# Performance work log

Measured on AMD Instinct MI355X. Metric: run time of the kernel, lower is better.

The kernel has to match this reference:

```python
import jax, jax.numpy as jnp
import numpy as np

B, T, F, H, L = 256, 512, 64, 256, 2
DH = 2 * H          # decoder hidden size (bidirectional encoder concat)
OUT, OSL = 2, 20    # output_size, output_seq_len


def gru_cell(x, h, Wih, Whh, bih, bhh):
    # PyTorch GRU cell, gate order (r, z, n)
    gi = x @ Wih.T + bih
    gh = h @ Whh.T + bhh
    ir, iz, inn = jnp.split(gi, 3, axis=-1)
    hr, hz, hn = jnp.split(gh, 3, axis=-1)
    r = jax.nn.sigmoid(ir + hr)
    z = jax.nn.sigmoid(iz + hz)
    n = jnp.tanh(inn + r * hn)
    return (1.0 - z) * n + z * h


def setup_inputs() -> dict:
    key = jax.random.key(0)
    ks = iter(jax.random.split(key, 32))
    def p(shape, scale=0.05):
        return jax.random.normal(next(ks), shape, dtype=jnp.float32) * scale
    inp = {
        "x": p((B, T, F), 1.0),
        "start_token": jnp.zeros((1, 1, OUT), jnp.float32),
        # encoder layer 0 (input F), layer 1 (input 2H); axis 0 = direction (fwd, bwd)
        "enc_Wih0": p((2, 3 * H, F)), "enc_Whh0": p((2, 3 * H, H)),
        "enc_bih0": p((2, 3 * H)),   "enc_bhh0": p((2, 3 * H)),
        "enc_Wih1": p((2, 3 * H, 2 * H)), "enc_Whh1": p((2, 3 * H, H)),
        "enc_bih1": p((2, 3 * H)),   "enc_bhh1": p((2, 3 * H)),
        # decoder: unidirectional, hidden DH; layer0 input OUT, layer1 input DH
        "dec_Wih0": p((3 * DH, OUT)), "dec_Whh0": p((3 * DH, DH)),
        "dec_bih0": p((3 * DH,)),    "dec_bhh0": p((3 * DH,)),
        "dec_Wih1": p((3 * DH, DH)), "dec_Whh1": p((3 * DH, DH)),
        "dec_bih1": p((3 * DH,)),    "dec_bhh1": p((3 * DH,)),
        "fc_W": p((OUT, DH)), "fc_b": p((OUT,)),
    }
    return inp


def _run_dir(xs, Wih, Whh, bih, bhh, reverse):
    # xs: [T, B, Fin] -> (ys [T, B, H], h_T [B, H])
    h0 = jnp.zeros((xs.shape[1], Whh.shape[1]), xs.dtype)
    def step(h, xt):
        hn = gru_cell(xt, h, Wih, Whh, bih, bhh)
        return hn, hn
    hT, ys = jax.lax.scan(step, h0, xs, reverse=reverse)
    return ys, hT


def reference(x, start_token,
              enc_Wih0, enc_Whh0, enc_bih0, enc_bhh0,
              enc_Wih1, enc_Whh1, enc_bih1, enc_bhh1,
              dec_Wih0, dec_Whh0, dec_bih0, dec_bhh0,
              dec_Wih1, dec_Whh1, dec_bih1, dec_bhh1,
              fc_W, fc_b):
    b = x.shape[0]
    xs = jnp.swapaxes(x, 0, 1)  # [T, B, F]
    enc_layers = [(enc_Wih0, enc_Whh0, enc_bih0, enc_bhh0),
                  (enc_Wih1, enc_Whh1, enc_bih1, enc_bhh1)]
    hiddens = []
    layer_in = xs
    for (Wih, Whh, bih, bhh) in enc_layers:
        yf, hf = _run_dir(layer_in, Wih[0], Whh[0], bih[0], bhh[0], reverse=False)
        yb, hb = _run_dir(layer_in, Wih[1], Whh[1], bih[1], bhh[1], reverse=True)
        layer_in = jnp.concatenate([yf, yb], axis=-1)   # [T, B, 2H]
        hiddens.append(jnp.concatenate([hf, hb], axis=-1))  # [B, 2H] = cat(fwd, bwd)
    inp0 = jnp.broadcast_to(start_token, (b, 1, OUT))[:, 0]  # [B, OUT]
    def dec_step(carry, _):
        inp, (h0, h1) = carry
        h0n = gru_cell(inp, h0, dec_Wih0, dec_Whh0, dec_bih0, dec_bhh0)
        h1n = gru_cell(h0n, h1, dec_Wih1, dec_Whh1, dec_bih1, dec_bhh1)
        pred = h1n @ fc_W.T + fc_b
        return (pred, (h0n, h1n)), pred
    _, preds = jax.lax.scan(dec_step, (inp0, (hiddens[0], hiddens[1])), None, length=OSL)
    return jnp.swapaxes(preds, 0, 1)  # [B, OSL, OUT]
```

## Files before the change

kernel.cpp:

```cpp
#include <hip/hip_runtime.h>
#include <hip/hip_bf16.h>
#include <stdint.h>
#include <stddef.h>


typedef __bf16 bf16_t;
typedef bf16_t bf16x8 __attribute__((ext_vector_type(8)));
typedef float  f32x4  __attribute__((ext_vector_type(4)));

#define B_   256
#define T_   512
#define F_   64
#define H_   256
#define G_   768
#define DH_  512
#define DG_  1536
#define OSL_ 20

__device__ __forceinline__ float sigm(float x) {
    float e = __builtin_amdgcn_exp2f(-1.442695040888963f * x);
    return __builtin_amdgcn_rcpf(1.0f + e);
}
__device__ __forceinline__ float tanh_(float x) {
    float e = __builtin_amdgcn_exp2f(-2.885390081777927f * x);
    return __builtin_amdgcn_rcpf(1.0f + e) * 2.0f - 1.0f;
}

__device__ __forceinline__ bf16x8 load_f32x8_as_bf16(const float* p) {
    f32x4 u = *(const f32x4*)p;
    f32x4 v = *(const f32x4*)(p + 4);
    bf16x8 r;
    r[0]=(bf16_t)u[0]; r[1]=(bf16_t)u[1]; r[2]=(bf16_t)u[2]; r[3]=(bf16_t)u[3];
    r[4]=(bf16_t)v[0]; r[5]=(bf16_t)v[1]; r[6]=(bf16_t)v[2]; r[7]=(bf16_t)v[3];
    return r;
}

__global__ __launch_bounds__(256) void prep_all(
    const float* __restrict__ s0, const float* __restrict__ s1,
    const float* __restrict__ s2, const float* __restrict__ s3,
    const float* __restrict__ s4, const float* __restrict__ s5,
    const float* __restrict__ s6,
    bf16_t* __restrict__ d0, bf16_t* __restrict__ d1, bf16_t* __restrict__ d2,
    bf16_t* __restrict__ d3, bf16_t* __restrict__ d4, bf16_t* __restrict__ d5,
    bf16_t* __restrict__ d6,
    const float* __restrict__ wih0d, const float* __restrict__ fcw,
    const float* __restrict__ fcb, const float* __restrict__ bih0d,
    const float* __restrict__ st, bf16_t* __restrict__ weff,
    float* __restrict__ beff, float* __restrict__ ov,
    unsigned int* __restrict__ bar) {
    int i = blockIdx.x * 256 + threadIdx.x;
    switch (blockIdx.y) {
      case 0: if (i < 2*G_*F_)  d0[i] = (bf16_t)s0[i]; break;
      case 1: if (i < 2*G_*H_)  d1[i] = (bf16_t)s1[i]; break;
      case 2: if (i < 2*G_*DH_) d2[i] = (bf16_t)s2[i]; break;
      case 3: if (i < 2*G_*H_)  d3[i] = (bf16_t)s3[i]; break;
      case 4: if (i < DG_*DH_)  d4[i] = (bf16_t)s4[i]; break;
      case 5: if (i < DG_*DH_)  d5[i] = (bf16_t)s5[i]; break;
      case 6: if (i < DG_*DH_)  d6[i] = (bf16_t)s6[i]; break;
      default: {
        if (i < 1024) bar[i] = 0u;
        if (i < DG_*DH_) {
          int g = i >> 9, k = i & 511;
          float a0 = wih0d[g * 2], a1 = wih0d[g * 2 + 1];
          weff[i] = (bf16_t)(a0 * fcw[k] + a1 * fcw[DH_ + k]);
          if (k == 0) {
            beff[g] = a0 * fcb[0] + a1 * fcb[1] + bih0d[g];
            ov[g]   = a0 * st[0]  + a1 * st[1]  + bih0d[g];
          }
        }
      } break;
    }
}

__global__ __launch_bounds__(256) void gemm_gi(
    const float* __restrict__ x, const bf16_t* __restrict__ xcat,
    const bf16_t* __restrict__ Bt, bf16_t* __restrict__ gi, int t0, int K) {
    __shared__ bf16_t As[128 * 64];
    __shared__ bf16_t Bs[128 * 64];
    int m0 = blockIdx.x * 128, n0 = blockIdx.y * 128;
    int tid = threadIdx.x;
    int lane = tid & 63, w = tid >> 6;
    int col = lane & 15, quad = lane >> 4;
    int qm = (w >> 1) * 64, qn = (w & 1) * 64;

    int tl = m0 >> 8;
    int bbase = m0 & 255;
    int t_real = t0 + tl;
    if (n0 >= 768) t_real = (T_ - 1) - t_real;

    f32x4 acc[4][4] = {};
    for (int k0 = 0; k0 < K; k0 += 64) {
        __syncthreads();
#pragma unroll
        for (int i = 0; i < 4; i++) {
            int c = i * 256 + tid;
            int m = c >> 3, kc = c & 7;
            int kcs = kc ^ (m & 7);
            bf16x8 av;
            if (K == 64) {
                av = load_f32x8_as_bf16(x + ((size_t)(bbase + m) * T_ + t_real) * F_ + kcs * 8);
            } else {
                av = *(const bf16x8*)(xcat + ((size_t)t_real * B_ + bbase + m) * DH_ + k0 + kcs * 8);
            }
            *(bf16x8*)(&As[c * 8]) = av;
            *(bf16x8*)(&Bs[c * 8]) = *(const bf16x8*)(Bt + (size_t)(n0 + m) * K + k0 + kcs * 8);
        }
        __syncthreads();
#pragma unroll
        for (int kt = 0; kt < 2; kt++) {
            bf16x8 a[4], b[4];
#pragma unroll
            for (int mt = 0; mt < 4; mt++) {
                int r = qm + mt * 16 + col;
                a[mt] = *(const bf16x8*)(&As[(r * 8 + ((kt * 4 + quad) ^ (r & 7))) * 8]);
                int rn = qn + mt * 16 + col;
                b[mt] = *(const bf16x8*)(&Bs[(rn * 8 + ((kt * 4 + quad) ^ (rn & 7))) * 8]);
            }
#pragma unroll
            for (int mt = 0; mt < 4; mt++)
#pragma unroll
                for (int nt = 0; nt < 4; nt++)
                    acc[mt][nt] = __builtin_amdgcn_mfma_f32_16x16x32_bf16(a[mt], b[nt], acc[mt][nt], 0, 0, 0);
        }
    }
#pragma unroll
    for (int mt = 0; mt < 4; mt++)
#pragma unroll
        for (int nt = 0; nt < 4; nt++)
#pragma unroll
            for (int i = 0; i < 4; i++) {
                int row = m0 + qm + mt * 16 + quad * 4 + i;
                int cg  = n0 + qn + nt * 16 + col;
                gi[(size_t)row * DG_ + cg] = (bf16_t)acc[mt][nt][i];
            }
}

__global__ __launch_bounds__(512) void gru_scan(
    const bf16_t* __restrict__ gi, int t0, int tc,
    const bf16_t* __restrict__ whh,
    const float* __restrict__ bih, const float* __restrict__ bhh,
    float* __restrict__ hstate, bf16_t* __restrict__ y, float* __restrict__ hT) {
    __shared__ bf16_t gi_lds[16 * 768];
    __shared__ bf16_t h_lds[2 * 16 * 264];

    int dir = blockIdx.x >> 4;
    int b0  = (blockIdx.x & 15) * 16;
    int tid = threadIdx.x;
    int w = tid >> 6, lane = tid & 63, col = lane & 15, quad = lane >> 4;

    bf16x8 wf[3][2][8];
    const bf16_t* wbase = whh + (size_t)dir * G_ * H_;
#pragma unroll
    for (int g = 0; g < 3; g++)
#pragma unroll
        for (int nt = 0; nt < 2; nt++) {
            int row = g * 256 + w * 32 + nt * 16 + col;
#pragma unroll
            for (int kt = 0; kt < 8; kt++)
                wf[g][nt][kt] = *(const bf16x8*)(wbase + (size_t)row * H_ + kt * 32 + quad * 8);
        }
    float brz[2][2], bin_[2], bhn[2];
#pragma unroll
    for (int nt = 0; nt < 2; nt++) {
        int j = w * 32 + nt * 16 + col;
        brz[0][nt] = bih[dir * G_ + j] + bhh[dir * G_ + j];
        brz[1][nt] = bih[dir * G_ + 256 + j] + bhh[dir * G_ + 256 + j];
        bin_[nt]   = bih[dir * G_ + 512 + j];
        bhn[nt]    = bhh[dir * G_ + 512 + j];
    }
    int bb[3], oo[3];
#pragma unroll
    for (int it = 0; it < 3; it++) {
        int c = it * 512 + tid;
        bb[it] = c / 96;
        oo[it] = (c % 96) * 8;
    }
    float hold[2][4];
#pragma unroll
    for (int nt = 0; nt < 2; nt++)
#pragma unroll
        for (int i = 0; i < 4; i++) {
            int j = w * 32 + nt * 16 + col;
            hold[nt][i] = t0 ? hstate[dir * 65536 + (b0 + quad * 4 + i) * 256 + j] : 0.0f;
        }
    for (int i = tid; i < 16 * 264; i += 512) {
        int b = i / 264, j = i % 264;
        float v = (t0 && j < 256) ? hstate[dir * 65536 + (b0 + b) * 256 + j] : 0.0f;
        h_lds[i] = (bf16_t)v;
    }
#pragma unroll
    for (int it = 0; it < 3; it++) {
        int c = it * 512 + tid;
        *(bf16x8*)(&gi_lds[c * 8]) =
            *(const bf16x8*)(gi + ((size_t)0 * B_ + b0 + bb[it]) * DG_ + dir * G_ + oo[it]);
    }
    __syncthreads();

    for (int s = 0; s < tc; s++) {
        int par = s & 1;
        int t = t0 + s;
        int sn = (s + 1 < tc) ? (s + 1) : s;

        bf16x8 pg[3];
#pragma unroll
        for (int it = 0; it < 3; it++)
            pg[it] = *(const bf16x8*)(gi + ((size_t)sn * B_ + b0 + bb[it]) * DG_ + dir * G_ + oo[it]);

        f32x4 acc[3][2] = {};
        const bf16_t* hcur = &h_lds[par * 4224];
#pragma unroll
        for (int kt = 0; kt < 8; kt++) {
            bf16x8 af = *(const bf16x8*)(hcur + col * 264 + kt * 32 + quad * 8);
#pragma unroll
            for (int g = 0; g < 3; g++)
#pragma unroll
                for (int nt = 0; nt < 2; nt++)
                    acc[g][nt] = __builtin_amdgcn_mfma_f32_16x16x32_bf16(af, wf[g][nt][kt], acc[g][nt], 0, 0, 0);
        }

        bf16_t* hnext = &h_lds[(par ^ 1) * 4224];
        int tp = dir ? (T_ - 1 - t) : t;
#pragma unroll
        for (int nt = 0; nt < 2; nt++) {
            int j = w * 32 + nt * 16 + col;
#pragma unroll
            for (int i = 0; i < 4; i++) {
                int b = quad * 4 + i;
                float gr = acc[0][nt][i] + (float)gi_lds[b * 768 + j]       + brz[0][nt];
                float gz = acc[1][nt][i] + (float)gi_lds[b * 768 + 256 + j] + brz[1][nt];
                float gn = (float)gi_lds[b * 768 + 512 + j] + bin_[nt];
                float r = sigm(gr), z = sigm(gz);
                float n = tanh_(gn + r * (acc[2][nt][i] + bhn[nt]));
                float hv = (1.0f - z) * n + z * hold[nt][i];
                hold[nt][i] = hv;
                hnext[b * 264 + j] = (bf16_t)hv;
                if (y) y[((size_t)tp * B_ + b0 + b) * DH_ + dir * H_ + j] = (bf16_t)hv;
                if (t == T_ - 1) hT[(size_t)(b0 + b) * DH_ + dir * H_ + j] = hv;
            }
        }
        __syncthreads();
#pragma unroll
        for (int it = 0; it < 3; it++)
            *(bf16x8*)(&gi_lds[(it * 512 + tid) * 8]) = pg[it];
        __syncthreads();
    }
#pragma unroll
    for (int nt = 0; nt < 2; nt++)
#pragma unroll
        for (int i = 0; i < 4; i++) {
            int j = w * 32 + nt * 16 + col;
            hstate[dir * 65536 + (b0 + quad * 4 + i) * 256 + j] = hold[nt][i];
        }
}


__device__ __forceinline__ void gbar(unsigned int* cnt) {
    __syncthreads();
    if (threadIdx.x == 0) {
        __hip_atomic_fetch_add(cnt, 1u, __ATOMIC_RELAXED, __HIP_MEMORY_SCOPE_AGENT);
        unsigned int s = 0;
        while (__hip_atomic_load(cnt, __ATOMIC_RELAXED, __HIP_MEMORY_SCOPE_AGENT) < 8u
               && ++s < (1u << 20))
            __builtin_amdgcn_s_sleep(1);
    }
    __syncthreads();
}

__device__ __forceinline__ void stage16_x(bf16_t* lds, const bf16_t* src) {
    f32x4 v0, v1, v2, v3;
    const char* s = (const char*)src;
    const char* a0 = s + threadIdx.x * 16;
    asm volatile(
        "global_load_dwordx4 %0, %4, off sc0 sc1\n\t"
        "global_load_dwordx4 %1, %5, off sc0 sc1\n\t"
        "global_load_dwordx4 %2, %6, off sc0 sc1\n\t"
        "global_load_dwordx4 %3, %7, off sc0 sc1\n\t"
        "s_waitcnt vmcnt(0)"
        : "=&v"(v0), "=&v"(v1), "=&v"(v2), "=&v"(v3)
        : "v"(a0), "v"(a0 + 4096), "v"(a0 + 8192), "v"(a0 + 12288)
        : "memory");
    f32x4 vv[4] = { v0, v1, v2, v3 };
#pragma unroll
    for (int i2 = 0; i2 < 4; ++i2) {
        int off = i2 * 4096 + threadIdx.x * 16;
        int row = off >> 10;
        int swz = off ^ ((row & 7) << 4);
        *(f32x4*)((char*)lds + swz) = vv[i2];
    }
}

__device__ __forceinline__ bf16x8 fragrd(const bf16_t* lds, int kt, int col, int quad) {
    int byte = (col * 1024 + kt * 64 + quad * 16) ^ ((col & 7) << 4);
    return *(const bf16x8*)((const char*)lds + byte);
}

__device__ __forceinline__ void publish(bf16_t* dst, int b, int j, float hv, int col) {
    bf16_t hb = (bf16_t)hv;
    unsigned short mb;
    __builtin_memcpy(&mb, &hb, 2);
    unsigned int pv = (unsigned int)__shfl_xor((int)(unsigned int)mb, 1);
    if ((col & 1) == 0) {
        unsigned int word = (unsigned int)mb | (pv << 16);
        void* addr = (char*)dst + (size_t)(b * DH_ + j) * 2;
        asm volatile("global_store_dword %0, %1, off sc0 sc1"
                     :: "v"(addr), "v"(word) : "memory");
    }
}

__device__ __forceinline__ void cell_step(
    const bf16_t* sh, const bf16_t* sx, bool dox,
    const bf16_t* __restrict__ Wx, const bf16_t* __restrict__ Wh,
    int j, int col, int quad, int grp,
    float br, float bz, float bin_, float bhn,
    float hold[4], bf16_t* hout, float* hist_t) {
    f32x4 aR = {}, aZ = {}, aIN = {}, aHN = {};
#pragma unroll
    for (int kt = 0; kt < 16; ++kt) {
        bf16x8 ah = fragrd(sh, kt, col, quad);
        bf16x8 w0 = *(const bf16x8*)(Wh + (size_t)j * DH_ + kt * 32 + quad * 8);
        bf16x8 w1 = *(const bf16x8*)(Wh + (size_t)(DH_ + j) * DH_ + kt * 32 + quad * 8);
        bf16x8 w2 = *(const bf16x8*)(Wh + (size_t)(2 * DH_ + j) * DH_ + kt * 32 + quad * 8);
        aR  = __builtin_amdgcn_mfma_f32_16x16x32_bf16(ah, w0, aR, 0, 0, 0);
        aZ  = __builtin_amdgcn_mfma_f32_16x16x32_bf16(ah, w1, aZ, 0, 0, 0);
        aHN = __builtin_amdgcn_mfma_f32_16x16x32_bf16(ah, w2, aHN, 0, 0, 0);
        if (dox) {
            bf16x8 ax = fragrd(sx, kt, col, quad);
            bf16x8 x0 = *(const bf16x8*)(Wx + (size_t)j * DH_ + kt * 32 + quad * 8);
            bf16x8 x1 = *(const bf16x8*)(Wx + (size_t)(DH_ + j) * DH_ + kt * 32 + quad * 8);
            bf16x8 x2 = *(const bf16x8*)(Wx + (size_t)(2 * DH_ + j) * DH_ + kt * 32 + quad * 8);
            aR  = __builtin_amdgcn_mfma_f32_16x16x32_bf16(ax, x0, aR, 0, 0, 0);
            aZ  = __builtin_amdgcn_mfma_f32_16x16x32_bf16(ax, x1, aZ, 0, 0, 0);
            aIN = __builtin_amdgcn_mfma_f32_16x16x32_bf16(ax, x2, aIN, 0, 0, 0);
        }
    }
#pragma unroll
    for (int i = 0; i < 4; ++i) {
        int b = grp * 16 + quad * 4 + i;
        float r = sigm(aR[i] + br);
        float z = sigm(aZ[i] + bz);
        float n = tanh_(aIN[i] + bin_ + r * (aHN[i] + bhn));
        float hv = (1.0f - z) * n + z * hold[i];
        hold[i] = hv;
        if (hist_t) hist_t[(size_t)b * DH_ + j] = hv;
        publish(hout, b, j, hv, col);
    }
}

__global__ __launch_bounds__(256) void dec_persist(
    const bf16_t* __restrict__ weff, const float* __restrict__ beff,
    const float* __restrict__ ov,
    const bf16_t* __restrict__ wdhh0, const float* __restrict__ dbhh0,
    const bf16_t* __restrict__ wdih1, const float* __restrict__ dbih1,
    const bf16_t* __restrict__ wdhh1, const float* __restrict__ dbhh1,
    const float* __restrict__ h0init, const float* __restrict__ h1init,
    bf16_t* hx00, bf16_t* hx01, bf16_t* hx10, bf16_t* hx11,
    float* __restrict__ hist, unsigned int* __restrict__ bar) {
    __shared__ bf16_t sh[16 * 512];
    __shared__ bf16_t sx[16 * 512];
    int jblk = blockIdx.x & 7;
    int grp  = blockIdx.x >> 3;
    int tid = threadIdx.x, w = tid >> 6, lane = tid & 63;
    int col = lane & 15, quad = lane >> 4;
    int j = jblk * 64 + w * 16 + col;

    float b0r = beff[j] + dbhh0[j],           b0z = beff[DH_ + j] + dbhh0[DH_ + j];
    float b0in = beff[2 * DH_ + j],           b0hn = dbhh0[2 * DH_ + j];
    float o0r = ov[j] + dbhh0[j],             o0z = ov[DH_ + j] + dbhh0[DH_ + j];
    float o0in = ov[2 * DH_ + j];
    float b1r = dbih1[j] + dbhh1[j],          b1z = dbih1[DH_ + j] + dbhh1[DH_ + j];
    float b1in = dbih1[2 * DH_ + j],          b1hn = dbhh1[2 * DH_ + j];

    float hold0[4], hold1[4];
#pragma unroll
    for (int i = 0; i < 4; ++i) {
        int b = grp * 16 + quad * 4 + i;
        float v0 = h0init[(size_t)b * DH_ + j];
        float v1 = h1init[(size_t)b * DH_ + j];
        hold0[i] = v0; hold1[i] = v1;
        publish(hx01, b, j, v0, col);
        publish(hx11, b, j, v1, col);
    }
    gbar(bar + grp);

    int ph = 1;
    for (int t = 0; t < OSL_; ++t) {
        bf16_t* write0 = (t & 1) ? hx01 : hx00;
        bf16_t* read0  = (t & 1) ? hx00 : hx01;
        bf16_t* write1 = (t & 1) ? hx11 : hx10;
        bf16_t* read1  = (t & 1) ? hx10 : hx11;
        bool dox0 = (t > 0);

        if (t == 0) stage16_x(sh, read0 + (size_t)grp * 16 * DH_);
        stage16_x(sx, read1 + (size_t)grp * 16 * DH_);
        __syncthreads();
        cell_step(sh, sx, dox0, weff, wdhh0, j, col, quad, grp,
                  dox0 ? b0r : o0r, dox0 ? b0z : o0z, dox0 ? b0in : o0in, b0hn,
                  hold0, write0, nullptr);
        gbar(bar + ph * 16 + grp); ph++;

        stage16_x(sh, write0 + (size_t)grp * 16 * DH_);
        __syncthreads();
        cell_step(sx, sh, true, wdih1, wdhh1, j, col, quad, grp,
                  b1r, b1z, b1in, b1hn,
                  hold1, write1, hist + (size_t)t * B_ * DH_);
        if (t < OSL_ - 1) { gbar(bar + ph * 16 + grp); ph++; }
    }
}

__global__ __launch_bounds__(256) void fc_all(
    const float* __restrict__ hist, const float* __restrict__ fcw,
    const float* __restrict__ fcb, float* __restrict__ out) {
    int t  = blockIdx.x >> 4;
    int b0 = (blockIdx.x & 15) * 16;
    int tid = threadIdx.x;
    int bl = tid >> 4, o = (tid >> 3) & 1, part = tid & 7;
    const float* hp = hist + ((size_t)t * B_ + b0 + bl) * DH_;
    const float* wp = fcw + o * DH_;
    float s = 0.0f;
    for (int k = part * 64; k < part * 64 + 64; k += 4) {
        f32x4 hv = *(const f32x4*)(hp + k);
        f32x4 wv = *(const f32x4*)(wp + k);
        s += hv[0] * wv[0] + hv[1] * wv[1] + hv[2] * wv[2] + hv[3] * wv[3];
    }
    s += __shfl_down(s, 4); s += __shfl_down(s, 2); s += __shfl_down(s, 1);
    if (part == 0) out[(size_t)(b0 + bl) * (OSL_ * 2) + t * 2 + o] = s + fcb[o];
}


#define OFF_WIH0E 0ull
#define OFF_WHH0E 196608ull
#define OFF_WIH1E 983040ull
#define OFF_WHH1E 2555904ull
#define OFF_WDHH0 3342336ull
#define OFF_WDIH1 4915200ull
#define OFF_WDHH1 6488064ull
#define OFF_WEFF  8060928ull
#define OFF_BEFF  9633792ull
#define OFF_BAR   9641984ull
#define OFF_OV    9658368ull
#define OFF_H0A   9682944ull
#define OFF_H0B   10207232ull
#define OFF_H1A   10731520ull
#define OFF_H1B   11255808ull
#define OFF_HST   11780096ull
#define OFF_HIST  12304384ull
#define OFF_XCAT  22790144ull
#define OFF_GI    157007872ull

extern "C" void kernel_launch(void* const* d_in, const int* in_sizes, int n_in,
                              void* d_out, int out_size, void* d_ws, size_t ws_size,
                              hipStream_t stream) {
    const float* x      = (const float*)d_in[0];
    const float* st     = (const float*)d_in[1];
    const float* eWih0  = (const float*)d_in[2];
    const float* eWhh0  = (const float*)d_in[3];
    const float* ebih0  = (const float*)d_in[4];
    const float* ebhh0  = (const float*)d_in[5];
    const float* eWih1  = (const float*)d_in[6];
    const float* eWhh1  = (const float*)d_in[7];
    const float* ebih1  = (const float*)d_in[8];
    const float* ebhh1  = (const float*)d_in[9];
    const float* dWih0  = (const float*)d_in[10];
    const float* dWhh0  = (const float*)d_in[11];
    const float* dbih0  = (const float*)d_in[12];
    const float* dbhh0  = (const float*)d_in[13];
    const float* dWih1  = (const float*)d_in[14];
    const float* dWhh1  = (const float*)d_in[15];
    const float* dbih1  = (const float*)d_in[16];
    const float* dbhh1  = (const float*)d_in[17];
    const float* fcW    = (const float*)d_in[18];
    const float* fcb    = (const float*)d_in[19];

    char* ws = (char*)d_ws;
    bf16_t* wih0e = (bf16_t*)(ws + OFF_WIH0E);
    bf16_t* whh0e = (bf16_t*)(ws + OFF_WHH0E);
    bf16_t* wih1e = (bf16_t*)(ws + OFF_WIH1E);
    bf16_t* whh1e = (bf16_t*)(ws + OFF_WHH1E);
    bf16_t* wdhh0 = (bf16_t*)(ws + OFF_WDHH0);
    bf16_t* wdih1 = (bf16_t*)(ws + OFF_WDIH1);
    bf16_t* wdhh1 = (bf16_t*)(ws + OFF_WDHH1);
    bf16_t* weff  = (bf16_t*)(ws + OFF_WEFF);
    float*  beff  = (float*)(ws + OFF_BEFF);
    unsigned int* bar = (unsigned int*)(ws + OFF_BAR);
    float*  ovp   = (float*)(ws + OFF_OV);
    float*  h0init = (float*)(ws + OFF_H0A);
    float*  h1init = (float*)(ws + OFF_H1A);
    bf16_t* hx00  = (bf16_t*)(ws + OFF_H0B);
    bf16_t* hx01  = (bf16_t*)(ws + OFF_H0B + 262144ull);
    bf16_t* hx10  = (bf16_t*)(ws + OFF_H1B);
    bf16_t* hx11  = (bf16_t*)(ws + OFF_H1B + 262144ull);
    float*  hstate = (float*)(ws + OFF_HST);
    float*  hist  = (float*)(ws + OFF_HIST);
    bf16_t* xcat  = (bf16_t*)(ws + OFF_XCAT);
    bf16_t* gi    = (bf16_t*)(ws + OFF_GI);

    int Tc = 512;
    while (Tc > 8 && OFF_GI + (unsigned long long)Tc * 786432ull > (unsigned long long)ws_size)
        Tc >>= 1;
    int nch = T_ / Tc;

    prep_all<<<dim3(3072, 8), 256, 0, stream>>>(
        eWih0, eWhh0, eWih1, eWhh1, dWhh0, dWih1, dWhh1,
        wih0e, whh0e, wih1e, whh1e, wdhh0, wdih1, wdhh1,
        dWih0, fcW, fcb, dbih0, st, weff, beff, ovp, bar);

    for (int c = 0; c < nch; c++) {
        gemm_gi<<<dim3(Tc * 2, 12), 256, 0, stream>>>(x, nullptr, wih0e, gi, c * Tc, 64);
        gru_scan<<<32, 512, 0, stream>>>(gi, c * Tc, Tc, whh0e, ebih0, ebhh0, hstate, xcat, h0init);
    }
    for (int c = 0; c < nch; c++) {
        gemm_gi<<<dim3(Tc * 2, 12), 256, 0, stream>>>(nullptr, xcat, wih1e, gi, c * Tc, 512);
        gru_scan<<<32, 512, 0, stream>>>(gi, c * Tc, Tc, whh1e, ebih1, ebhh1, hstate, nullptr, h1init);
    }

    dec_persist<<<128, 256, 0, stream>>>(weff, beff, ovp,
                                         wdhh0, dbhh0, wdih1, dbih1, wdhh1, dbhh1,
                                         h0init, h1init,
                                         hx00, hx01, hx10, hx11,
                                         hist, bar);

    fc_all<<<OSL_ * 16, 256, 0, stream>>>(hist, fcW, fcb, (float*)d_out);
}
```

Measured before the change: 4.631 ms.

## Hold decoder weights in registers and split gates across waves in persistent decoder

The persistent decoder kernel now runs 256 blocks of 512 threads. Each block owns 32 hidden columns, and each wave preloads one gate/matrix weight slice into registers once, instead of re-reading the weights from global memory on every step. Partial MFMA results are exchanged through LDS, and two waves apply the gate nonlinearities. The group barrier now expects 16 blocks per batch group. This trades global weight traffic per step for high register pressure (48 bf16x8 fragments per thread), extra LDS exchanges and syncs, and more blocks joining each barrier, with only 2 of 8 waves doing the elementwise work.

```diff
diff --git a/kernel.cpp b/kernel.cpp
--- a/kernel.cpp
+++ b/kernel.cpp
@@ -254,38 +254,39 @@
 }
 
 
-__device__ __forceinline__ void gbar(unsigned int* cnt) {
+__device__ __forceinline__ void gbar16(unsigned int* cnt) {
     __syncthreads();
     if (threadIdx.x == 0) {
         __hip_atomic_fetch_add(cnt, 1u, __ATOMIC_RELAXED, __HIP_MEMORY_SCOPE_AGENT);
         unsigned int s = 0;
-        while (__hip_atomic_load(cnt, __ATOMIC_RELAXED, __HIP_MEMORY_SCOPE_AGENT) < 8u
+        while (__hip_atomic_load(cnt, __ATOMIC_RELAXED, __HIP_MEMORY_SCOPE_AGENT) < 16u
                && ++s < (1u << 20))
             __builtin_amdgcn_s_sleep(1);
     }
     __syncthreads();
 }
 
-__device__ __forceinline__ void stage16_x(bf16_t* lds, const bf16_t* src) {
-    f32x4 v0, v1, v2, v3;
-    const char* s = (const char*)src;
-    const char* a0 = s + threadIdx.x * 16;
+__device__ __forceinline__ void stage16v(bf16_t* lds, const bf16_t* src) {
+    f32x4 v0, v1;
+    const char* a0 = (const char*)src + threadIdx.x * 16;
     asm volatile(
-        "global_load_dwordx4 %0, %4, off sc0 sc1\n\t"
-        "global_load_dwordx4 %1, %5, off sc0 sc1\n\t"
-        "global_load_dwordx4 %2, %6, off sc0 sc1\n\t"
-        "global_load_dwordx4 %3, %7, off sc0 sc1\n\t"
+        "global_load_dwordx4 %0, %2, off sc0 sc1\n\t"
+        "global_load_dwordx4 %1, %3, off sc0 sc1\n\t"
         "s_waitcnt vmcnt(0)"
-        : "=&v"(v0), "=&v"(v1), "=&v"(v2), "=&v"(v3)
-        : "v"(a0), "v"(a0 + 4096), "v"(a0 + 8192), "v"(a0 + 12288)
+        : "=&v"(v0), "=&v"(v1)
+        : "v"(a0), "v"(a0 + 8192)
         : "memory");
-    f32x4 vv[4] = { v0, v1, v2, v3 };
-#pragma unroll
-    for (int i2 = 0; i2 < 4; ++i2) {
-        int off = i2 * 4096 + threadIdx.x * 16;
+    {
+        int off = threadIdx.x * 16;
         int row = off >> 10;
         int swz = off ^ ((row & 7) << 4);
-        *(f32x4*)((char*)lds + swz) = vv[i2];
+        *(f32x4*)((char*)lds + swz) = v0;
+    }
+    {
+        int off = 8192 + threadIdx.x * 16;
+        int row = off >> 10;
+        int swz = off ^ ((row & 7) << 4);
+        *(f32x4*)((char*)lds + swz) = v1;
     }
 }
 
@@ -307,46 +308,7 @@
     }
 }
 
-__device__ __forceinline__ void cell_step(
-    const bf16_t* sh, const bf16_t* sx, bool dox,
-    const bf16_t* __restrict__ Wx, const bf16_t* __restrict__ Wh,
-    int j, int col, int quad, int grp,
-    float br, float bz, float bin_, float bhn,
-    float hold[4], bf16_t* hout, float* hist_t) {
-    f32x4 aR = {}, aZ = {}, aIN = {}, aHN = {};
-#pragma unroll
-    for (int kt = 0; kt < 16; ++kt) {
-        bf16x8 ah = fragrd(sh, kt, col, quad);
-        bf16x8 w0 = *(const bf16x8*)(Wh + (size_t)j * DH_ + kt * 32 + quad * 8);
-        bf16x8 w1 = *(const bf16x8*)(Wh + (size_t)(DH_ + j) * DH_ + kt * 32 + quad * 8);
-        bf16x8 w2 = *(const bf16x8*)(Wh + (size_t)(2 * DH_ + j) * DH_ + kt * 32 + quad * 8);
-        aR  = __builtin_amdgcn_mfma_f32_16x16x32_bf16(ah, w0, aR, 0, 0, 0);
-        aZ  = __builtin_amdgcn_mfma_f32_16x16x32_bf16(ah, w1, aZ, 0, 0, 0);
-        aHN = __builtin_amdgcn_mfma_f32_16x16x32_bf16(ah, w2, aHN, 0, 0, 0);
-        if (dox) {
-            bf16x8 ax = fragrd(sx, kt, col, quad);
-            bf16x8 x0 = *(const bf16x8*)(Wx + (size_t)j * DH_ + kt * 32 + quad * 8);
-            bf16x8 x1 = *(const bf16x8*)(Wx + (size_t)(DH_ + j) * DH_ + kt * 32 + quad * 8);
-            bf16x8 x2 = *(const bf16x8*)(Wx + (size_t)(2 * DH_ + j) * DH_ + kt * 32 + quad * 8);
-            aR  = __builtin_amdgcn_mfma_f32_16x16x32_bf16(ax, x0, aR, 0, 0, 0);
-            aZ  = __builtin_amdgcn_mfma_f32_16x16x32_bf16(ax, x1, aZ, 0, 0, 0);
-            aIN = __builtin_amdgcn_mfma_f32_16x16x32_bf16(ax, x2, aIN, 0, 0, 0);
-        }
-    }
-#pragma unroll
-    for (int i = 0; i < 4; ++i) {
-        int b = grp * 16 + quad * 4 + i;
-        float r = sigm(aR[i] + br);
-        float z = sigm(aZ[i] + bz);
-        float n = tanh_(aIN[i] + bin_ + r * (aHN[i] + bhn));
-        float hv = (1.0f - z) * n + z * hold[i];
-        hold[i] = hv;
-        if (hist_t) hist_t[(size_t)b * DH_ + j] = hv;
-        publish(hout, b, j, hv, col);
-    }
-}
-
-__global__ __launch_bounds__(256) void dec_persist(
+__global__ __launch_bounds__(512, 2) void dec_persist(
     const bf16_t* __restrict__ weff, const float* __restrict__ beff,
     const float* __restrict__ ov,
     const bf16_t* __restrict__ wdhh0, const float* __restrict__ dbhh0,
@@ -357,30 +319,52 @@
     float* __restrict__ hist, unsigned int* __restrict__ bar) {
     __shared__ bf16_t sh[16 * 512];
     __shared__ bf16_t sx[16 * 512];
-    int jblk = blockIdx.x & 7;
-    int grp  = blockIdx.x >> 3;
+    __shared__ f32x4 exch[12 * 64];
+
+    int s  = blockIdx.x & 15;
+    int g  = blockIdx.x >> 4;
+    int js = s * 32;
     int tid = threadIdx.x, w = tid >> 6, lane = tid & 63;
     int col = lane & 15, quad = lane >> 4;
-    int j = jblk * 64 + w * 16 + col;
-
-    float b0r = beff[j] + dbhh0[j],           b0z = beff[DH_ + j] + dbhh0[DH_ + j];
-    float b0in = beff[2 * DH_ + j],           b0hn = dbhh0[2 * DH_ + j];
-    float o0r = ov[j] + dbhh0[j],             o0z = ov[DH_ + j] + dbhh0[DH_ + j];
-    float o0in = ov[2 * DH_ + j];
-    float b1r = dbih1[j] + dbhh1[j],          b1z = dbih1[DH_ + j] + dbhh1[DH_ + j];
-    float b1in = dbih1[2 * DH_ + j],          b1hn = dbhh1[2 * DH_ + j];
+
+    const bf16_t* mats[4] = { wdhh0, weff, wdih1, wdhh1 };
+    bf16x8 frg[3][16];
+    int tmat[3], texch[3];
+#pragma unroll
+    for (int sl = 0; sl < 3; ++sl) {
+        int idx = w + sl * 8;
+        int m = idx / 6, rem = idx - m * 6;
+        int gate = rem >> 1, jh = rem & 1;
+        tmat[sl] = m;
+        texch[sl] = (m & 1) * 6 + rem;
+        int row = gate * 512 + js + jh * 16 + col;
+        const bf16_t* M = mats[m];
+#pragma unroll
+        for (int kt = 0; kt < 16; ++kt)
+            frg[sl][kt] = *(const bf16x8*)(M + (size_t)row * DH_ + kt * 32 + quad * 8);
+    }
+
+    int je = js + (w & 1) * 16 + col;
+    float b0r = beff[je] + dbhh0[je],        b0z = beff[DH_ + je] + dbhh0[DH_ + je];
+    float b0in = beff[2 * DH_ + je],         b0hn = dbhh0[2 * DH_ + je];
+    float o0r = ov[je] + dbhh0[je],          o0z = ov[DH_ + je] + dbhh0[DH_ + je];
+    float o0in = ov[2 * DH_ + je];
+    float b1r = dbih1[je] + dbhh1[je],       b1z = dbih1[DH_ + je] + dbhh1[DH_ + je];
+    float b1in = dbih1[2 * DH_ + je],        b1hn = dbhh1[2 * DH_ + je];
 
     float hold0[4], hold1[4];
-#pragma unroll
-    for (int i = 0; i < 4; ++i) {
-        int b = grp * 16 + quad * 4 + i;
-        float v0 = h0init[(size_t)b * DH_ + j];
-        float v1 = h1init[(size_t)b * DH_ + j];
-        hold0[i] = v0; hold1[i] = v1;
-        publish(hx01, b, j, v0, col);
-        publish(hx11, b, j, v1, col);
-    }
-    gbar(bar + grp);
+    if (w < 2) {
+#pragma unroll
+        for (int i = 0; i < 4; ++i) {
+            int b = g * 16 + quad * 4 + i;
+            float v0 = h0init[(size_t)b * DH_ + je];
+            float v1 = h1init[(size_t)b * DH_ + je];
+            hold0[i] = v0; hold1[i] = v1;
+            publish(hx01, b, je, v0, col);
+            publish(hx11, b, je, v1, col);
+        }
+    }
+    gbar16(bar + g);
 
     int ph = 1;
     for (int t = 0; t < OSL_; ++t) {
@@ -388,22 +372,106 @@
         bf16_t* read0  = (t & 1) ? hx00 : hx01;
         bf16_t* write1 = (t & 1) ? hx11 : hx10;
         bf16_t* read1  = (t & 1) ? hx10 : hx11;
-        bool dox0 = (t > 0);
-
-        if (t == 0) stage16_x(sh, read0 + (size_t)grp * 16 * DH_);
-        stage16_x(sx, read1 + (size_t)grp * 16 * DH_);
-        __syncthreads();
-        cell_step(sh, sx, dox0, weff, wdhh0, j, col, quad, grp,
-                  dox0 ? b0r : o0r, dox0 ? b0z : o0z, dox0 ? b0in : o0in, b0hn,
-                  hold0, write0, nullptr);
-        gbar(bar + ph * 16 + grp); ph++;
-
-        stage16_x(sh, write0 + (size_t)grp * 16 * DH_);
-        __syncthreads();
-        cell_step(sx, sh, true, wdih1, wdhh1, j, col, quad, grp,
-                  b1r, b1z, b1in, b1hn,
-                  hold1, write1, hist + (size_t)t * B_ * DH_);
-        if (t < OSL_ - 1) { gbar(bar + ph * 16 + grp); ph++; }
+        bool dox = (t > 0);
+
+        if (t == 0) stage16v(sh, read0 + (size_t)g * 16 * DH_);
+        stage16v(sx, read1 + (size_t)g * 16 * DH_);
+        __syncthreads();
+
+        {
+            f32x4 acc[3] = {};
+#pragma unroll
+            for (int sl = 0; sl < 3; ++sl) {
+                if (tmat[sl] == 0) {
+#pragma unroll
+                    for (int kt = 0; kt < 16; ++kt)
+                        acc[sl] = __builtin_amdgcn_mfma_f32_16x16x32_bf16(
+                            fragrd(sh, kt, col, quad), frg[sl][kt], acc[sl], 0, 0, 0);
+                } else if (tmat[sl] == 1 && dox) {
+#pragma unroll
+                    for (int kt = 0; kt < 16; ++kt)
+                        acc[sl] = __builtin_amdgcn_mfma_f32_16x16x32_bf16(
+                            fragrd(sx, kt, col, quad), frg[sl][kt], acc[sl], 0, 0, 0);
+                }
+            }
+#pragma unroll
+            for (int sl = 0; sl < 3; ++sl)
+                if (tmat[sl] <= 1) exch[texch[sl] * 64 + lane] = acc[sl];
+        }
+        __syncthreads();
+
+        if (w < 2) {
+            int jh = w;
+            f32x4 aR0 = exch[(0 + jh) * 64 + lane];
+            f32x4 aZ0 = exch[(2 + jh) * 64 + lane];
+            f32x4 aN0 = exch[(4 + jh) * 64 + lane];
+            f32x4 aR1 = {}, aZ1 = {}, aN1 = {};
+            if (dox) {
+                aR1 = exch[(6 + jh) * 64 + lane];
+                aZ1 = exch[(8 + jh) * 64 + lane];
+                aN1 = exch[(10 + jh) * 64 + lane];
+            }
+#pragma unroll
+            for (int i = 0; i < 4; ++i) {
+                int b = g * 16 + quad * 4 + i;
+                float r = sigm(aR0[i] + aR1[i] + (dox ? b0r : o0r));
+                float z = sigm(aZ0[i] + aZ1[i] + (dox ? b0z : o0z));
+                float gin = dox ? (aN1[i] + b0in) : o0in;
+                float n = tanh_(gin + r * (aN0[i] + b0hn));
+                float hv = (1.0f - z) * n + z * hold0[i];
+                hold0[i] = hv;
+                publish(write0, b, je, hv, col);
+            }
+        }
+        gbar16(bar + ph * 16 + g); ph++;
+
+        stage16v(sh, write0 + (size_t)g * 16 * DH_);
+        __syncthreads();
+
+        {
+            f32x4 acc[3] = {};
+#pragma unroll
+            for (int sl = 0; sl < 3; ++sl) {
+                if (tmat[sl] == 2) {
+#pragma unroll
+                    for (int kt = 0; kt < 16; ++kt)
+                        acc[sl] = __builtin_amdgcn_mfma_f32_16x16x32_bf16(
+                            fragrd(sh, kt, col, quad), frg[sl][kt], acc[sl], 0, 0, 0);
+                } else if (tmat[sl] == 3) {
+#pragma unroll
+                    for (int kt = 0; kt < 16; ++kt)
+                        acc[sl] = __builtin_amdgcn_mfma_f32_16x16x32_bf16(
+                            fragrd(sx, kt, col, quad), frg[sl][kt], acc[sl], 0, 0, 0);
+                }
+            }
+#pragma unroll
+            for (int sl = 0; sl < 3; ++sl)
+                if (tmat[sl] >= 2) exch[texch[sl] * 64 + lane] = acc[sl];
+        }
+        __syncthreads();
+
+        if (w < 2) {
+            int jh = w;
+            f32x4 giR = exch[(0 + jh) * 64 + lane];
+            f32x4 giZ = exch[(2 + jh) * 64 + lane];
+            f32x4 giN = exch[(4 + jh) * 64 + lane];
+            f32x4 ghR = exch[(6 + jh) * 64 + lane];
+            f32x4 ghZ = exch[(8 + jh) * 64 + lane];
+            f32x4 ghN = exch[(10 + jh) * 64 + lane];
+            float* hist_t = hist + (size_t)t * B_ * DH_;
+#pragma unroll
+            for (int i = 0; i < 4; ++i) {
+                int b = g * 16 + quad * 4 + i;
+                float r = sigm(giR[i] + ghR[i] + b1r);
+                float z = sigm(giZ[i] + ghZ[i] + b1z);
+                float n = tanh_(giN[i] + b1in + r * (ghN[i] + b1hn));
+                float hv = (1.0f - z) * n + z * hold1[i];
+                hold1[i] = hv;
+                hist_t[(size_t)b * DH_ + je] = hv;
+                publish(write1, b, je, hv, col);
+            }
+        }
+        if (t < OSL_ - 1) { gbar16(bar + ph * 16 + g); ph++; }
     }
 }
 
@@ -513,7 +581,7 @@
         gru_scan<<<32, 512, 0, stream>>>(gi, c * Tc, Tc, whh1e, ebih1, ebhh1, hstate, nullptr, h1init);
     }
 
-    dec_persist<<<128, 256, 0, stream>>>(weff, beff, ovp,
+    dec_persist<<<256, 512, 0, stream>>>(weff, beff, ovp,
                                          wdhh0, dbhh0, wdih1, dbih1, wdhh1, dbhh1,
                                          h0init, h1init,
                                          hx00, hx01, hx10, hx11,
```

Result: no change. 4.611 ms (-0.4%).
